# Performance work log

Measured on AMD Instinct MI355X. Metric: run time of the kernel, lower is better.

## Reference

```python
import jax, jax.numpy as jnp
import numpy as np

B, T, E, K, NNEG = 128, 512, 128, 4, 64


def setup_inputs() -> dict:
    key = jax.random.key(0)
    k1, k2, k3, k4 = jax.random.split(key, 4)
    base_payload = jax.random.normal(k1, (B, T, E), dtype=jnp.float32)
    mapped_ctx_payload = jax.random.normal(k2, (B, T, E, K), dtype=jnp.float32)
    seq_lens = jax.random.randint(k3, (B,), 1, T + 1, dtype=jnp.int32)
    # valid positions mask over the flattened (B*T) pool of possible negatives
    valid = (jnp.arange(T)[None, :] < seq_lens[:, None]).reshape(-1)  # [B*T]
    logits = jnp.where(valid, 0.0, -1e30)[None, :]                    # [1, B*T]
    logits = jnp.broadcast_to(logits, (B, B * T))
    # mirrors torch.multinomial(mask, n_negatives): one draw set per batch row
    sample_ids = jax.random.categorical(k4, logits, shape=(NNEG, B)).T.astype(jnp.int32)
    return {
        "base_payload": base_payload,
        "mapped_ctx_payload": mapped_ctx_payload,
        "seq_lens": seq_lens,
        "sample_ids": sample_ids,
    }


def reference(base_payload, mapped_ctx_payload, seq_lens, sample_ids):
    b, t, e = base_payload.shape
    n_steps = mapped_ctx_payload.shape[-1]
    # length mask [b, t]
    len_mask = (jnp.arange(t)[None, :] < seq_lens[:, None]).astype(base_payload.dtype)
    # zero context embeddings past each sequence's length
    trimmed_mce = mapped_ctx_payload * len_mask[:, :, None, None]  # [b, t, e, n_steps]
    # gather sampled negatives from the flattened base embedding pool
    neg_samples = base_payload.reshape(b * t, e)[sample_ids]  # [b, n_neg, e]

    step_losses = []
    for i in range(1, n_steps + 1):
        ce_i = trimmed_mce[:, : t - i, :, i - 1]   # [b, t-i, e]
        be_i = base_payload[:, i:]                  # [b, t-i, e]
        positive_pred = jnp.sum(ce_i * be_i, axis=-1)             # [b, t-i]
        neg_pred = jnp.einsum('bse,bne->bsn', ce_i, neg_samples)  # [b, t-i, n_neg]
        logits = jnp.concatenate([positive_pred[..., None], neg_pred], axis=-1)
        step_losses.append(-jax.nn.log_softmax(logits, axis=-1)[:, :, 0].mean())
    return jnp.stack(step_losses).mean()
```

## Files before the change

kernel.cpp:

```cpp
#include <hip/hip_runtime.h>
#include <math.h>

#define NB 128
#define NT 512
#define NEDIM 128
#define NNEG 64
#define SCHUNK 32
#define NBLK (NB * (NT / SCHUNK))

typedef __bf16 bf16x8 __attribute__((ext_vector_type(8)));
typedef float  f32x4  __attribute__((ext_vector_type(4)));

__launch_bounds__(256, 3)
__global__ void cpc_mfma_kernel(const float* __restrict__ base,
                                const float* __restrict__ mce,
                                const int*  __restrict__ seq_lens,
                                const int*  __restrict__ sample_ids,
                                float* __restrict__ ws)
{
    const int j  = blockIdx.x;
    const int b  = j >> 3;
    const int c0 = (j & 7) * 2;
    const int L  = seq_lens[b];
    const float LOG65 = 4.1743873f;
    const float wgt[4] = {1.f/261632.f, 1.f/261120.f, 1.f/260608.f, 1.f/260096.f};

    const int tid  = threadIdx.x;
    const int lane = tid & 63;
    const int w    = tid >> 6;
    const int q    = lane >> 4;
    const int fl   = lane & 15;

    auto masked_const = [&](int s0) {
        float c = 0.f;
        #pragma unroll
        for (int i = 1; i <= 4; ++i) {
            int hi = min(SCHUNK, (NT - i) - s0);
            if (hi > 0) c += (float)hi * LOG65 * wgt[i - 1];
        }
        return c;
    };

    if (c0 * SCHUNK >= L) {
        if (tid == 0) {
            ws[b * 16 + c0]     = masked_const(c0 * SCHUNK);
            ws[b * 16 + c0 + 1] = masked_const((c0 + 1) * SCHUNK);
        }
        return;
    }

    __shared__ __bf16 Afrag[2048 * 8];
    __shared__ __bf16 Bfrag[1024 * 8];
    __shared__ float  pos_lds[128];
    __shared__ float  wsum[4];

    const float4* mce4 = (const float4*)mce;

    {
        int n = tid & 63;
        int r = sample_ids[b * NNEG + n];
        const float4* srcb = (const float4*)(base + (size_t)r * NEDIM);
        int eb0 = (tid >> 6) * 4;
        #pragma unroll
        for (int it = 0; it < 4; ++it) {
            int eb = eb0 + it;
            float4 v0 = srcb[eb * 2], v1 = srcb[eb * 2 + 1];
            const float* f0 = (const float*)&v0;
            const float* f1 = (const float*)&v1;
            bf16x8 o;
            #pragma unroll
            for (int u = 0; u < 4; ++u) { o[u] = (__bf16)f0[u]; o[4 + u] = (__bf16)f1[u]; }
            *(bf16x8*)(&Bfrag[(eb * 64 + n) * 8]) = o;
        }
    }

    for (int t = 0; t < 2; ++t) {
        const int c    = c0 + t;
        const int s0   = c * SCHUNK;
        const int slot = b * 16 + c;

        if (s0 >= L) {
            if (tid == 0) ws[slot] = masked_const(s0);
            continue;
        }

        #pragma unroll
        for (int it = 0; it < 2; ++it) {
            int g  = tid + 256 * it;
            int s  = g & 31;
            int eb = g >> 5;
            const float4* src = mce4 + (size_t)(b * NT + s0 + s) * NEDIM + eb * 8;
            float4 v[8];
            #pragma unroll
            for (int u = 0; u < 8; ++u) v[u] = src[u];
            const float* vf = (const float*)v;
            int Cs = (eb >> 2) * 8 + (s >> 2);
            int base_chunk = Cs * 64 + (eb & 3) * 16 + (s & 3) * 4;
            int x = Cs & 7;
            #pragma unroll
            for (int k = 0; k < 4; ++k) {
                int phys = (base_chunk + k) ^ x;
                bf16x8 o;
                #pragma unroll
                for (int u = 0; u < 8; ++u) o[u] = (__bf16)vf[4 * u + k];
                *(bf16x8*)(&Afrag[phys * 8]) = o;
            }
        }
        __syncthreads();

        f32x4 acc[2][4];
        #pragma unroll
        for (int mtl = 0; mtl < 2; ++mtl)
            #pragma unroll
            for (int nt = 0; nt < 4; ++nt) acc[mtl][nt] = (f32x4){0.f, 0.f, 0.f, 0.f};

        #pragma unroll
        for (int kstep = 0; kstep < 4; ++kstep) {
            bf16x8 af[2];
            #pragma unroll
            for (int mtl = 0; mtl < 2; ++mtl) {
                int Cs = kstep * 8 + (2 * w + mtl);
                int phys = (Cs * 64 + lane) ^ (Cs & 7);
                af[mtl] = *(const bf16x8*)(&Afrag[phys * 8]);
            }
            bf16x8 bv[4];
            #pragma unroll
            for (int nt = 0; nt < 4; ++nt) {
                int cB = (kstep * 4 + q) * 64 + nt * 16 + fl;
                bv[nt] = *(const bf16x8*)(&Bfrag[cB * 8]);
            }
            #pragma unroll
            for (int mtl = 0; mtl < 2; ++mtl)
                #pragma unroll
                for (int nt = 0; nt < 4; ++nt)
                    acc[mtl][nt] = __builtin_amdgcn_mfma_f32_16x16x32_bf16(
                        af[mtl], bv[nt], acc[mtl][nt], 0, 0, 0);
        }

        {
            int m    = tid >> 1;
            int eh   = tid & 1;
            int sloc = m >> 2, ip = (m & 3) + 1;
            int srow = s0 + sloc + ip; if (srow > NT - 1) srow = NT - 1;
            const float4* brow4 = (const float4*)(base + (size_t)(b * NT + srow) * NEDIM + eh * 64);
            int mt = m >> 4, flm = m & 15;
            float psum = 0.f;
            #pragma unroll
            for (int el = 0; el < 8; ++el) {
                int eb = eh * 8 + el;
                int Cs = (eb >> 2) * 8 + mt;
                int phys = (Cs * 64 + (eb & 3) * 16 + flm) ^ (Cs & 7);
                bf16x8 av = *(const bf16x8*)(&Afrag[phys * 8]);
                float4 b0 = brow4[el * 2], b1 = brow4[el * 2 + 1];
                const float* f0 = (const float*)&b0;
                const float* f1 = (const float*)&b1;
                #pragma unroll
                for (int u = 0; u < 4; ++u) {
                    psum = fmaf((float)av[u],     f0[u], psum);
                    psum = fmaf((float)av[4 + u], f1[u], psum);
                }
            }
            psum += __shfl_xor(psum, 1);
            if (eh == 0) pos_lds[m] = psum;
        }
        __syncthreads();

        float lossacc = 0.f;
        #pragma unroll
        for (int mtl = 0; mtl < 2; ++mtl) {
            #pragma unroll
            for (int r = 0; r < 4; ++r) {
                int m  = w * 32 + mtl * 16 + q * 4 + r;
                int sg = s0 + (m >> 2);
                int ip = (m & 3) + 1;
                float z0 = acc[mtl][0][r], z1 = acc[mtl][1][r];
                float z2 = acc[mtl][2][r], z3 = acc[mtl][3][r];
                float p  = pos_lds[m];
                float mx = fmaxf(fmaxf(z0, z1), fmaxf(z2, z3));
                mx = fmaxf(mx, __shfl_xor(mx, 1));
                mx = fmaxf(mx, __shfl_xor(mx, 2));
                mx = fmaxf(mx, __shfl_xor(mx, 4));
                mx = fmaxf(mx, __shfl_xor(mx, 8));
                mx = fmaxf(mx, p);
                float es = __expf(z0 - mx) + __expf(z1 - mx)
                         + __expf(z2 - mx) + __expf(z3 - mx);
                es += __shfl_xor(es, 1);
                es += __shfl_xor(es, 2);
                es += __shfl_xor(es, 4);
                es += __shfl_xor(es, 8);
                es += __expf(p - mx);
                float loss = __logf(es) + (mx - p);
                loss = (sg < L) ? loss : LOG65;
                bool take = (sg < NT - ip) && (fl == 0);
                lossacc += take ? wgt[ip - 1] * loss : 0.f;
            }
        }
        lossacc += __shfl_xor(lossacc, 16);
        lossacc += __shfl_xor(lossacc, 32);
        if (lane == 0) wsum[w] = lossacc;
        __syncthreads();
        if (tid == 0) ws[slot] = wsum[0] + wsum[1] + wsum[2] + wsum[3];
    }
}

__global__ void reduce_k(const float* __restrict__ ws, float* __restrict__ out) {
    const int tid = threadIdx.x;
    float s = 0.f;
    #pragma unroll
    for (int i = 0; i < NBLK / 256; ++i) s += ws[tid + 256 * i];
    s += __shfl_xor(s, 1);
    s += __shfl_xor(s, 2);
    s += __shfl_xor(s, 4);
    s += __shfl_xor(s, 8);
    s += __shfl_xor(s, 16);
    s += __shfl_xor(s, 32);
    __shared__ float wsum[4];
    if ((tid & 63) == 0) wsum[tid >> 6] = s;
    __syncthreads();
    if (tid == 0) out[0] = wsum[0] + wsum[1] + wsum[2] + wsum[3];
}

extern "C" void kernel_launch(void* const* d_in, const int* in_sizes, int n_in,
                              void* d_out, int out_size, void* d_ws, size_t ws_size,
                              hipStream_t stream) {
    (void)in_sizes; (void)n_in; (void)out_size; (void)ws_size;
    const float* base       = (const float*)d_in[0];
    const float* mce        = (const float*)d_in[1];
    const int*   seq_lens   = (const int*)d_in[2];
    const int*   sample_ids = (const int*)d_in[3];
    float* out = (float*)d_out;
    float* ws  = (float*)d_ws;

    cpc_mfma_kernel<<<dim3(NBLK / 2), 256, 0, stream>>>(base, mce, seq_lens, sample_ids, ws);
    reduce_k<<<1, 256, 0, stream>>>(ws, out);
}
```

Baseline: 228.5 us.

## Process four chunks per block with register prefetch of next chunk

Each block now handles four 32-row sequence chunks instead of two, halving the grid and amortizing the negative-sample B-fragment load over more chunks. The next chunk's context-embedding tile is prefetched into registers right after the LDS write barrier, so global loads overlap the MFMA and softmax work of the current chunk. Fully masked chunks are filled with the constant loss up front. In exchange, register pressure rises (launch bounds lowered to 2 blocks per SM) and there are fewer blocks to spread across the GPU.

After: 225.3 us. No clear change (-1.4%).

```diff
diff --git a/kernel.cpp b/kernel.cpp
--- a/kernel.cpp
+++ b/kernel.cpp
@@ -11,7 +11,7 @@
 typedef __bf16 bf16x8 __attribute__((ext_vector_type(8)));
 typedef float  f32x4  __attribute__((ext_vector_type(4)));
 
-__launch_bounds__(256, 3)
+__launch_bounds__(256, 2)
 __global__ void cpc_mfma_kernel(const float* __restrict__ base,
                                 const float* __restrict__ mce,
                                 const int*  __restrict__ seq_lens,
@@ -19,8 +19,8 @@
                                 float* __restrict__ ws)
 {
     const int j  = blockIdx.x;
-    const int b  = j >> 3;
-    const int c0 = (j & 7) * 2;
+    const int b  = j >> 2;
+    const int c0 = (j & 3) * 4;
     const int L  = seq_lens[b];
     const float LOG65 = 4.1743873f;
     const float wgt[4] = {1.f/261632.f, 1.f/261120.f, 1.f/260608.f, 1.f/260096.f};
@@ -41,13 +41,13 @@
         return c;
     };
 
-    if (c0 * SCHUNK >= L) {
-        if (tid == 0) {
-            ws[b * 16 + c0]     = masked_const(c0 * SCHUNK);
-            ws[b * 16 + c0 + 1] = masked_const((c0 + 1) * SCHUNK);
-        }
-        return;
+    int rem  = L - c0 * SCHUNK;
+    int nact = rem <= 0 ? 0 : min(4, (rem + SCHUNK - 1) >> 5);
+    if (tid == 0) {
+        for (int c = c0 + nact; c < c0 + 4; ++c)
+            ws[b * 16 + c] = masked_const(c * SCHUNK);
     }
+    if (nact == 0) return;
 
     __shared__ __bf16 Afrag[2048 * 8];
     __shared__ __bf16 Bfrag[1024 * 8];
@@ -74,26 +74,32 @@
         }
     }
 
-    for (int t = 0; t < 2; ++t) {
-        const int c    = c0 + t;
-        const int s0   = c * SCHUNK;
-        const int slot = b * 16 + c;
-
-        if (s0 >= L) {
-            if (tid == 0) ws[slot] = masked_const(s0);
-            continue;
-        }
-
+    float4 pf[2][8];
+    auto load_pf = [&](int c) {
+        int s0l = c * SCHUNK;
         #pragma unroll
         for (int it = 0; it < 2; ++it) {
             int g  = tid + 256 * it;
             int s  = g & 31;
             int eb = g >> 5;
-            const float4* src = mce4 + (size_t)(b * NT + s0 + s) * NEDIM + eb * 8;
-            float4 v[8];
-            #pragma unroll
-            for (int u = 0; u < 8; ++u) v[u] = src[u];
-            const float* vf = (const float*)v;
+            const float4* src = mce4 + (size_t)(b * NT + s0l + s) * NEDIM + eb * 8;
+            #pragma unroll
+            for (int u = 0; u < 8; ++u) pf[it][u] = src[u];
+        }
+    };
+    load_pf(c0);
+
+    for (int t = 0; t < nact; ++t) {
+        const int c    = c0 + t;
+        const int s0   = c * SCHUNK;
+        const int slot = b * 16 + c;
+
+        #pragma unroll
+        for (int it = 0; it < 2; ++it) {
+            int g  = tid + 256 * it;
+            int s  = g & 31;
+            int eb = g >> 5;
+            const float* vf = (const float*)pf[it];
             int Cs = (eb >> 2) * 8 + (s >> 2);
             int base_chunk = Cs * 64 + (eb & 3) * 16 + (s & 3) * 4;
             int x = Cs & 7;
@@ -107,6 +113,8 @@
             }
         }
         __syncthreads();
+
+        if (t + 1 < nact) load_pf(c0 + t + 1);
 
         f32x4 acc[2][4];
         #pragma unroll
@@ -231,6 +239,6 @@
     float* out = (float*)d_out;
     float* ws  = (float*)d_ws;
 
-    cpc_mfma_kernel<<<dim3(NBLK / 2), 256, 0, stream>>>(base, mce, seq_lens, sample_ids, ws);
+    cpc_mfma_kernel<<<dim3(NBLK / 4), 256, 0, stream>>>(base, mce, seq_lens, sample_ids, ws);
     reduce_k<<<1, 256, 0, stream>>>(ws, out);
 }
```
